# Kernel tuning notes

Hardware: AMD Instinct MI355X
Metric: run time of the kernel (lower is better)

The kernel has to match this reference:

```python
import jax, jax.numpy as jnp
import numpy as np

N, C_IN, C_OUT, K, B, EMB, GROUPS, EPS = 131072, 64, 64, 27, 8, 512, 32, 1e-5


def octree_group_norm(x, batch_id, gamma, beta):
    # Per-sample, per-group stats over all nodes of that sample (nempty=False).
    n, c = x.shape
    cpg = c // GROUPS
    xg = x.reshape(n, GROUPS, cpg)
    cnt = jax.ops.segment_sum(jnp.ones((n,), x.dtype), batch_id, num_segments=B)  # [B]
    s = jax.ops.segment_sum(xg.sum(-1), batch_id, num_segments=B)                 # [B,G]
    ss = jax.ops.segment_sum((xg * xg).sum(-1), batch_id, num_segments=B)         # [B,G]
    denom = (cnt * cpg)[:, None]
    mean = s / denom
    var = ss / denom - mean * mean
    xn = (xg - mean[batch_id][:, :, None]) * jax.lax.rsqrt(var[batch_id][:, :, None] + EPS)
    return xn.reshape(n, c) * gamma + beta


def octree_conv(x, neigh, W, b):
    # Sparse 27-neighbor gather conv: gather [N,27,Cin], contract with [27,Cin,Cout].
    gathered = x[neigh]                                   # [N,K,Cin]
    return jnp.einsum('nkc,kco->no', gathered, W) + b


def setup_inputs() -> dict:
    key = jax.random.key(0)
    ks = jax.random.split(key, 12)
    return {
        'x': jax.random.normal(ks[0], (N, C_IN), jnp.float32),
        'time_emb': jax.random.normal(ks[1], (B, EMB), jnp.float32),
        'batch_id': jnp.sort(jax.random.randint(ks[2], (N,), 0, B)),
        'neigh': jax.random.randint(ks[3], (N, K), 0, N),
        'gn1_gamma': jnp.ones((C_IN,), jnp.float32),
        'gn1_beta': jnp.zeros((C_IN,), jnp.float32),
        'W1': jax.random.normal(ks[4], (K, C_IN, C_OUT), jnp.float32) * 0.05,
        'b1': jax.random.normal(ks[5], (C_OUT,), jnp.float32) * 0.01,
        'Wt': jax.random.normal(ks[6], (EMB, C_OUT), jnp.float32) * 0.04,
        'bt': jnp.zeros((C_OUT,), jnp.float32),
        'gn2_gamma': jnp.ones((C_OUT,), jnp.float32),
        'gn2_beta': jnp.zeros((C_OUT,), jnp.float32),
        'W2': jax.random.normal(ks[7], (K, C_OUT, C_OUT), jnp.float32) * 0.05,
        'b2': jnp.zeros((C_OUT,), jnp.float32),
    }


def reference(x, time_emb, batch_id, neigh, gn1_gamma, gn1_beta, W1, b1,
              Wt, bt, gn2_gamma, gn2_beta, W2, b2):
    h = jax.nn.silu(octree_group_norm(x, batch_id, gn1_gamma, gn1_beta))
    h = octree_conv(h, neigh, W1, b1)
    # time embedding: SiLU -> Linear, scattered per-sample onto nodes
    t = jax.nn.silu(time_emb) @ Wt + bt                   # [B, Cout]
    h = h + t[batch_id]
    h = jax.nn.silu(octree_group_norm(h, batch_id, gn2_gamma, gn2_beta))
    h = octree_conv(h, neigh, W2, b2)
    return h + x  # res_conv is identity since dim_in == dim_out
```

## Files before the change

kernel.cpp:

```cpp
#include <hip/hip_runtime.h>
#include <hip/hip_bf16.h>
#include <cstdint>

typedef unsigned short u16;
typedef __attribute__((ext_vector_type(8))) __bf16 bf16x8;
typedef __attribute__((ext_vector_type(4))) float f32x4;

#define N_NODES 131072
#define C 64
#define KNB 27
#define BATCH 8
#define EMB 512
#define NGROUP 32
#define GN_EPS 1e-5f

__device__ __forceinline__ void gload_lds16(const void* gsrc, void* ldsdst) {
    __builtin_amdgcn_global_load_lds(
        (const __attribute__((address_space(1))) char*)(unsigned long long)(uintptr_t)gsrc,
        (__attribute__((address_space(3))) char*)(unsigned int)(uintptr_t)ldsdst,
        16, 0, 0);
}

__device__ __forceinline__ float silu_f(float x) {
    return x / (1.0f + __expf(-x));
}

__device__ __forceinline__ u16 f2bf(float x) {
    __hip_bfloat16 h = __float2bfloat16(x);
    return __builtin_bit_cast(u16, h);
}

__device__ __forceinline__ float bf2f(u16 h) {
    unsigned u = ((unsigned)h) << 16;
    return __builtin_bit_cast(float, u);
}

__device__ __forceinline__ unsigned pack2(float a, float b) {
    return (unsigned)f2bf(a) | ((unsigned)f2bf(b) << 16);
}

__global__ void setup_kernel(const float* __restrict__ W1, const float* __restrict__ W2,
                             u16* __restrict__ Wb1, u16* __restrict__ Wb2,
                             const float* __restrict__ te, const float* __restrict__ Wt,
                             const float* __restrict__ bt, float* __restrict__ tvec,
                             const float* __restrict__ x, const int* __restrict__ batch_id,
                             float* __restrict__ stats, float* __restrict__ cnt) {
    __shared__ float sh[520];
    const int bid = blockIdx.x;
    const int t = threadIdx.x;
    if (bid < 216) {
        const int per = KNB * C * C;
        int e0 = (bid * 256 + t) * 4;
#pragma unroll
        for (int d = 0; d < 4; ++d) {
            int idx = e0 + d;
            const float* src = (idx < per) ? W1 : W2;
            u16* dst = (idx < per) ? Wb1 : Wb2;
            int e = (idx < per) ? idx : idx - per;
            int k = e >> 12;
            int rem = e & 4095;
            int co = rem >> 6;
            int ci = rem & 63;
            dst[e] = f2bf(src[(k * C + ci) * C + co]);
        }
    } else if (bid < 224) {
        int b = bid - 216;
        int co = t & 63, seg = t >> 6;
        float acc = 0.f;
        for (int i = 0; i < 128; ++i) {
            int e = seg * 128 + i;
            float v = te[b * EMB + e];
            acc += silu_f(v) * Wt[e * C + co];
        }
        sh[t] = acc;
        __syncthreads();
        if (t < 64) tvec[b * C + t] = sh[t] + sh[t + 64] + sh[t + 128] + sh[t + 192] + bt[t];
    } else {
        for (int i = t; i < 520; i += 256) sh[i] = 0.f;
        __syncthreads();
        const int n0 = (bid - 224) * 256;
        const int c4 = t & 15, r = t >> 4;
        float s0 = 0.f, ss0 = 0.f, s1 = 0.f, ss1 = 0.f, c = 0.f;
        int cur = -1;
        for (int i = 0; i < 16; ++i) {
            int n = n0 + i * 16 + r;
            int b = batch_id[n];
            if (b != cur) {
                if (cur >= 0) {
                    int g0 = 2 * c4;
                    atomicAdd(&sh[(cur * NGROUP + g0) * 2 + 0], s0);
                    atomicAdd(&sh[(cur * NGROUP + g0) * 2 + 1], ss0);
                    atomicAdd(&sh[(cur * NGROUP + g0 + 1) * 2 + 0], s1);
                    atomicAdd(&sh[(cur * NGROUP + g0 + 1) * 2 + 1], ss1);
                    if (c4 == 0) atomicAdd(&sh[512 + cur], c);
                }
                cur = b; s0 = ss0 = s1 = ss1 = c = 0.f;
            }
            float4 v = *(const float4*)(x + (size_t)n * C + c4 * 4);
            s0 += v.x + v.y;  ss0 += v.x * v.x + v.y * v.y;
            s1 += v.z + v.w;  ss1 += v.z * v.z + v.w * v.w;
            c += 1.f;
        }
        {
            int g0 = 2 * c4;
            atomicAdd(&sh[(cur * NGROUP + g0) * 2 + 0], s0);
            atomicAdd(&sh[(cur * NGROUP + g0) * 2 + 1], ss0);
            atomicAdd(&sh[(cur * NGROUP + g0 + 1) * 2 + 0], s1);
            atomicAdd(&sh[(cur * NGROUP + g0 + 1) * 2 + 1], ss1);
            if (c4 == 0) atomicAdd(&sh[512 + cur], c);
        }
        __syncthreads();
        for (int i = t; i < 512; i += 256)
            if (sh[i] != 0.f) atomicAdd(&stats[i], sh[i]);
        if (t < 8 && sh[512 + t] != 0.f) atomicAdd(&cnt[t], sh[512 + t]);
    }
}

__global__ void gn_apply_f32(const float* __restrict__ x, const int* __restrict__ batch_id,
                             const float* __restrict__ stats, const float* __restrict__ cnt,
                             const float* __restrict__ gamma, const float* __restrict__ beta,
                             u16* __restrict__ out) {
    int idx = blockIdx.x * 256 + threadIdx.x;
    int n = idx >> 3, seg = idx & 7;
    int b = batch_id[n];
    float denom = cnt[b] * 2.0f;
    float4 v0 = *(const float4*)(x + (size_t)n * C + seg * 8);
    float4 v1 = *(const float4*)(x + (size_t)n * C + seg * 8 + 4);
    float4 ga0 = *(const float4*)(gamma + seg * 8);
    float4 ga1 = *(const float4*)(gamma + seg * 8 + 4);
    float4 be0 = *(const float4*)(beta + seg * 8);
    float4 be1 = *(const float4*)(beta + seg * 8 + 4);
    float mn[4], rs[4];
#pragma unroll
    for (int p = 0; p < 4; ++p) {
        float2 st = *(const float2*)(stats + (b * NGROUP + seg * 4 + p) * 2);
        float mean = st.x / denom;
        float var = st.y / denom - mean * mean;
        mn[p] = mean;
        rs[p] = rsqrtf(var + GN_EPS);
    }
    float y0 = silu_f((v0.x - mn[0]) * rs[0] * ga0.x + be0.x);
    float y1 = silu_f((v0.y - mn[0]) * rs[0] * ga0.y + be0.y);
    float y2 = silu_f((v0.z - mn[1]) * rs[1] * ga0.z + be0.z);
    float y3 = silu_f((v0.w - mn[1]) * rs[1] * ga0.w + be0.w);
    float y4 = silu_f((v1.x - mn[2]) * rs[2] * ga1.x + be1.x);
    float y5 = silu_f((v1.y - mn[2]) * rs[2] * ga1.y + be1.y);
    float y6 = silu_f((v1.z - mn[3]) * rs[3] * ga1.z + be1.z);
    float y7 = silu_f((v1.w - mn[3]) * rs[3] * ga1.w + be1.w);
    uint4 o;
    o.x = pack2(y0, y1); o.y = pack2(y2, y3); o.z = pack2(y4, y5); o.w = pack2(y6, y7);
    *(uint4*)(out + (size_t)n * C + seg * 8) = o;
}

__global__ void gn_apply_bf16(const u16* __restrict__ x, const int* __restrict__ batch_id,
                              const float* __restrict__ stats, const float* __restrict__ cnt,
                              const float* __restrict__ gamma, const float* __restrict__ beta,
                              u16* __restrict__ out) {
    int idx = blockIdx.x * 256 + threadIdx.x;
    int n = idx >> 3, seg = idx & 7;
    int b = batch_id[n];
    float denom = cnt[b] * 2.0f;
    uint4 u = *(const uint4*)(x + (size_t)n * C + seg * 8);
    float4 ga0 = *(const float4*)(gamma + seg * 8);
    float4 ga1 = *(const float4*)(gamma + seg * 8 + 4);
    float4 be0 = *(const float4*)(beta + seg * 8);
    float4 be1 = *(const float4*)(beta + seg * 8 + 4);
    float mn[4], rs[4];
#pragma unroll
    for (int p = 0; p < 4; ++p) {
        float2 st = *(const float2*)(stats + (b * NGROUP + seg * 4 + p) * 2);
        float mean = st.x / denom;
        float var = st.y / denom - mean * mean;
        mn[p] = mean;
        rs[p] = rsqrtf(var + GN_EPS);
    }
    float v0 = bf2f(u.x & 0xffff), v1 = bf2f(u.x >> 16);
    float v2 = bf2f(u.y & 0xffff), v3 = bf2f(u.y >> 16);
    float v4 = bf2f(u.z & 0xffff), v5 = bf2f(u.z >> 16);
    float v6 = bf2f(u.w & 0xffff), v7 = bf2f(u.w >> 16);
    float y0 = silu_f((v0 - mn[0]) * rs[0] * ga0.x + be0.x);
    float y1 = silu_f((v1 - mn[0]) * rs[0] * ga0.y + be0.y);
    float y2 = silu_f((v2 - mn[1]) * rs[1] * ga0.z + be0.z);
    float y3 = silu_f((v3 - mn[1]) * rs[1] * ga0.w + be0.w);
    float y4 = silu_f((v4 - mn[2]) * rs[2] * ga1.x + be1.x);
    float y5 = silu_f((v5 - mn[2]) * rs[2] * ga1.y + be1.y);
    float y6 = silu_f((v6 - mn[3]) * rs[3] * ga1.z + be1.z);
    float y7 = silu_f((v7 - mn[3]) * rs[3] * ga1.w + be1.w);
    uint4 o;
    o.x = pack2(y0, y1); o.y = pack2(y2, y3); o.z = pack2(y4, y5); o.w = pack2(y6, y7);
    *(uint4*)(out + (size_t)n * C + seg * 8) = o;
}

template <bool ADD_T, bool FUSE_STATS, bool OUT_F32_RES>
__global__ __launch_bounds__(512, 4) void conv_kernel(
    const u16* __restrict__ act, const int* __restrict__ neigh,
    const u16* __restrict__ Wb, const float* __restrict__ bias,
    const float* __restrict__ tvec, const int* __restrict__ batch_id,
    const float* __restrict__ resid, void* __restrict__ outp,
    float* __restrict__ stats, float* __restrict__ cnt) {
    __shared__ u16 Wbuf[5 * 64 * 64];
    float* shs = (float*)Wbuf;

    const int tid = threadIdx.x;
    const int w = tid >> 6, lane = tid & 63;
    const int q = lane >> 4, m = lane & 15;
    const int n0 = blockIdx.x * 256;
    const int nw = n0 + w * 32;

    const int* nrow0 = neigh + (size_t)(nw + m) * KNB;
    const int* nrow1 = neigh + (size_t)(nw + 16 + m) * KNB;

    f32x4 acc[2][4] = {};
    bf16x8 aC[2][2];
    int offn0, offn1;

    {
        int o0 = nrow0[0] * C, o1 = nrow1[0] * C;
        aC[0][0] = *(const bf16x8*)(act + o0 + q * 8);
        aC[0][1] = *(const bf16x8*)(act + o0 + 32 + q * 8);
        aC[1][0] = *(const bf16x8*)(act + o1 + q * 8);
        aC[1][1] = *(const bf16x8*)(act + o1 + 32 + q * 8);
        offn0 = nrow0[1] * C;
        offn1 = nrow1[1] * C;
    }

    for (int phase = 0; phase < 6; ++phase) {
        const int k0 = phase * 5;
        const int nk = (phase == 5) ? 2 : 5;
        if (phase) __syncthreads();
        const int total = nk * 512;
#pragma unroll
        for (int it = 0; it < 5; ++it) {
            int cb = it * 512 + w * 64;
            if (cb < total) {
                int c = cb + lane;
                int r = c >> 3;
                int pos = c & 7;
                int srcc = pos ^ (r & 7);
                gload_lds16(Wb + (((k0 << 6) + r) << 6) + (srcc << 3), Wbuf + cb * 8);
            }
        }
        __syncthreads();

        for (int sI = 0; sI < nk; ++sI) {
            const int k = k0 + sI;
            const int kn = k + 1;
            bf16x8 an[2][2];
            if (kn < KNB) {
                an[0][0] = *(const bf16x8*)(act + offn0 + q * 8);
                an[0][1] = *(const bf16x8*)(act + offn0 + 32 + q * 8);
                an[1][0] = *(const bf16x8*)(act + offn1 + q * 8);
                an[1][1] = *(const bf16x8*)(act + offn1 + 32 + q * 8);
            }
            if (kn + 1 < KNB) {
                offn0 = nrow0[kn + 1] * C;
                offn1 = nrow1[kn + 1] * C;
            }
            const u16* wsl = Wbuf + sI * 4096;
#pragma unroll
            for (int kk = 0; kk < 2; ++kk) {
#pragma unroll
                for (int j = 0; j < 4; ++j) {
                    const int co = j * 16 + m;
                    const int lc = kk * 4 + q;
                    bf16x8 b = *(const bf16x8*)(wsl + (co << 6) + ((lc ^ (co & 7)) << 3));
                    acc[0][j] = __builtin_amdgcn_mfma_f32_16x16x32_bf16(aC[0][kk], b, acc[0][j], 0, 0, 0);
                    acc[1][j] = __builtin_amdgcn_mfma_f32_16x16x32_bf16(aC[1][kk], b, acc[1][j], 0, 0, 0);
                }
            }
            if (kn < KNB) {
                aC[0][0] = an[0][0]; aC[0][1] = an[0][1];
                aC[1][0] = an[1][0]; aC[1][1] = an[1][1];
            }
        }
    }

    float bs[4];
#pragma unroll
    for (int j = 0; j < 4; ++j) bs[j] = bias[j * 16 + m];

#pragma unroll
    for (int s = 0; s < 2; ++s) {
#pragma unroll
        for (int reg = 0; reg < 4; ++reg) {
            const int n = nw + s * 16 + q * 4 + reg;
            int b = 0;
            if (ADD_T) b = batch_id[n];
#pragma unroll
            for (int j = 0; j < 4; ++j) {
                const int co = j * 16 + m;
                float v = acc[s][j][reg] + bs[j];
                if (ADD_T) v += tvec[b * C + co];
                acc[s][j][reg] = v;
                if (OUT_F32_RES) {
                    ((float*)outp)[(size_t)n * C + co] = v + resid[(size_t)n * C + co];
                } else {
                    ((u16*)outp)[(size_t)n * C + co] = f2bf(v);
                }
            }
        }
    }

    if (FUSE_STATS) {
        __syncthreads();
        for (int i = tid; i < 520; i += 512) shs[i] = 0.f;
        __syncthreads();
        const int blo = batch_id[nw], bhi = batch_id[nw + 31];
        if (blo == bhi) {
#pragma unroll
            for (int j = 0; j < 4; ++j) {
                float s = 0.f, ss = 0.f;
#pragma unroll
                for (int sq = 0; sq < 2; ++sq)
#pragma unroll
                    for (int reg = 0; reg < 4; ++reg) {
                        float v = acc[sq][j][reg];
                        s += v; ss += v * v;
                    }
                s += __shfl_xor(s, 16, 64);  ss += __shfl_xor(ss, 16, 64);
                s += __shfl_xor(s, 32, 64);  ss += __shfl_xor(ss, 32, 64);
                s += __shfl_xor(s, 1, 64);   ss += __shfl_xor(ss, 1, 64);
                if (q == 0 && (m & 1) == 0) {
                    int g = (j * 16 + m) >> 1;
                    atomicAdd(&shs[(blo * NGROUP + g) * 2 + 0], s);
                    atomicAdd(&shs[(blo * NGROUP + g) * 2 + 1], ss);
                }
            }
        } else {
#pragma unroll
            for (int sq = 0; sq < 2; ++sq)
#pragma unroll
                for (int reg = 0; reg < 4; ++reg) {
                    int b = batch_id[nw + sq * 16 + q * 4 + reg];
#pragma unroll
                    for (int j = 0; j < 4; ++j) {
                        int g = (j * 16 + m) >> 1;
                        float v = acc[sq][j][reg];
                        atomicAdd(&shs[(b * NGROUP + g) * 2 + 0], v);
                        atomicAdd(&shs[(b * NGROUP + g) * 2 + 1], v * v);
                    }
                }
        }
        if (tid < 256) atomicAdd(&shs[512 + batch_id[n0 + tid]], 1.0f);
        __syncthreads();
        if (tid < 512 && shs[tid] != 0.f) atomicAdd(&stats[tid], shs[tid]);
        if (tid < 8 && shs[512 + tid] != 0.f) atomicAdd(&cnt[tid], shs[512 + tid]);
    }
}

extern "C" void kernel_launch(void* const* d_in, const int* in_sizes, int n_in,
                              void* d_out, int out_size, void* d_ws, size_t ws_size,
                              hipStream_t stream) {
    const float* x        = (const float*)d_in[0];
    const float* time_emb = (const float*)d_in[1];
    const int*   batch_id = (const int*)d_in[2];
    const int*   neigh    = (const int*)d_in[3];
    const float* g1       = (const float*)d_in[4];
    const float* be1      = (const float*)d_in[5];
    const float* W1       = (const float*)d_in[6];
    const float* b1       = (const float*)d_in[7];
    const float* Wt       = (const float*)d_in[8];
    const float* bt       = (const float*)d_in[9];
    const float* g2       = (const float*)d_in[10];
    const float* be2      = (const float*)d_in[11];
    const float* W2       = (const float*)d_in[12];
    const float* b2       = (const float*)d_in[13];

    char* ws = (char*)d_ws;
    u16*   h1     = (u16*)(ws + 0);
    u16*   h2     = (u16*)(ws + 16777216);
    u16*   h3     = (u16*)(ws + 33554432);
    u16*   Wb1    = (u16*)(ws + 50331648);
    u16*   Wb2    = (u16*)(ws + 50552832);
    float* tvec   = (float*)(ws + 50774016);
    float* stats1 = (float*)(ws + 50776064);
    float* cnt1   = stats1 + 512;
    float* stats2 = cnt1 + 8;
    float* cnt2   = stats2 + 512;

    hipMemsetAsync(ws + 50776064, 0, 1040 * sizeof(float), stream);
    setup_kernel<<<736, 256, 0, stream>>>(W1, W2, Wb1, Wb2, time_emb, Wt, bt, tvec,
                                          x, batch_id, stats1, cnt1);
    gn_apply_f32<<<4096, 256, 0, stream>>>(x, batch_id, stats1, cnt1, g1, be1, h1);
    conv_kernel<true, true, false><<<512, 512, 0, stream>>>(
        h1, neigh, Wb1, b1, tvec, batch_id, nullptr, (void*)h2, stats2, cnt2);
    gn_apply_bf16<<<4096, 256, 0, stream>>>(h2, batch_id, stats2, cnt2, g2, be2, h3);
    conv_kernel<false, false, true><<<512, 512, 0, stream>>>(
        h3, neigh, Wb2, b2, nullptr, nullptr, x, (void*)d_out, nullptr, nullptr);
}
```

Before: 302.6 us.

## Fuse all stages into one persistent kernel with grid barriers

Replaces the five separate launches (setup, two GN applies, two convs) with a single persistent 512-block kernel. Stages are separated by software grid barriers built on atomic counters. The conv gather is also deepened from double to triple-buffered register prefetch, with 6-tap weight phases and full unrolling. This removes launch gaps and inter-kernel drains, but relies on all 512 blocks being co-resident, adds spin-wait barrier costs, and raises register and LDS pressure.

Result: slower. 621.4 us (+105.4%).

```diff
diff --git a/kernel.cpp b/kernel.cpp
--- a/kernel.cpp
+++ b/kernel.cpp
@@ -6,13 +6,13 @@
 typedef __attribute__((ext_vector_type(8))) __bf16 bf16x8;
 typedef __attribute__((ext_vector_type(4))) float f32x4;
 
-#define N_NODES 131072
+#define NN 131072
 #define C 64
 #define KNB 27
-#define BATCH 8
 #define EMB 512
 #define NGROUP 32
 #define GN_EPS 1e-5f
+#define NBLK 512
 
 __device__ __forceinline__ void gload_lds16(const void* gsrc, void* ldsdst) {
     __builtin_amdgcn_global_load_lds(
@@ -39,168 +39,46 @@
     return (unsigned)f2bf(a) | ((unsigned)f2bf(b) << 16);
 }
 
-__global__ void setup_kernel(const float* __restrict__ W1, const float* __restrict__ W2,
-                             u16* __restrict__ Wb1, u16* __restrict__ Wb2,
-                             const float* __restrict__ te, const float* __restrict__ Wt,
-                             const float* __restrict__ bt, float* __restrict__ tvec,
-                             const float* __restrict__ x, const int* __restrict__ batch_id,
-                             float* __restrict__ stats, float* __restrict__ cnt) {
-    __shared__ float sh[520];
-    const int bid = blockIdx.x;
-    const int t = threadIdx.x;
-    if (bid < 216) {
-        const int per = KNB * C * C;
-        int e0 = (bid * 256 + t) * 4;
-#pragma unroll
-        for (int d = 0; d < 4; ++d) {
-            int idx = e0 + d;
-            const float* src = (idx < per) ? W1 : W2;
-            u16* dst = (idx < per) ? Wb1 : Wb2;
-            int e = (idx < per) ? idx : idx - per;
-            int k = e >> 12;
-            int rem = e & 4095;
-            int co = rem >> 6;
-            int ci = rem & 63;
-            dst[e] = f2bf(src[(k * C + ci) * C + co]);
-        }
-    } else if (bid < 224) {
-        int b = bid - 216;
-        int co = t & 63, seg = t >> 6;
-        float acc = 0.f;
-        for (int i = 0; i < 128; ++i) {
-            int e = seg * 128 + i;
-            float v = te[b * EMB + e];
-            acc += silu_f(v) * Wt[e * C + co];
-        }
-        sh[t] = acc;
-        __syncthreads();
-        if (t < 64) tvec[b * C + t] = sh[t] + sh[t + 64] + sh[t + 128] + sh[t + 192] + bt[t];
-    } else {
-        for (int i = t; i < 520; i += 256) sh[i] = 0.f;
-        __syncthreads();
-        const int n0 = (bid - 224) * 256;
-        const int c4 = t & 15, r = t >> 4;
-        float s0 = 0.f, ss0 = 0.f, s1 = 0.f, ss1 = 0.f, c = 0.f;
-        int cur = -1;
-        for (int i = 0; i < 16; ++i) {
-            int n = n0 + i * 16 + r;
-            int b = batch_id[n];
-            if (b != cur) {
-                if (cur >= 0) {
-                    int g0 = 2 * c4;
-                    atomicAdd(&sh[(cur * NGROUP + g0) * 2 + 0], s0);
-                    atomicAdd(&sh[(cur * NGROUP + g0) * 2 + 1], ss0);
-                    atomicAdd(&sh[(cur * NGROUP + g0 + 1) * 2 + 0], s1);
-                    atomicAdd(&sh[(cur * NGROUP + g0 + 1) * 2 + 1], ss1);
-                    if (c4 == 0) atomicAdd(&sh[512 + cur], c);
-                }
-                cur = b; s0 = ss0 = s1 = ss1 = c = 0.f;
-            }
-            float4 v = *(const float4*)(x + (size_t)n * C + c4 * 4);
-            s0 += v.x + v.y;  ss0 += v.x * v.x + v.y * v.y;
-            s1 += v.z + v.w;  ss1 += v.z * v.z + v.w * v.w;
-            c += 1.f;
-        }
-        {
-            int g0 = 2 * c4;
-            atomicAdd(&sh[(cur * NGROUP + g0) * 2 + 0], s0);
-            atomicAdd(&sh[(cur * NGROUP + g0) * 2 + 1], ss0);
-            atomicAdd(&sh[(cur * NGROUP + g0 + 1) * 2 + 0], s1);
-            atomicAdd(&sh[(cur * NGROUP + g0 + 1) * 2 + 1], ss1);
-            if (c4 == 0) atomicAdd(&sh[512 + cur], c);
-        }
-        __syncthreads();
-        for (int i = t; i < 512; i += 256)
-            if (sh[i] != 0.f) atomicAdd(&stats[i], sh[i]);
-        if (t < 8 && sh[512 + t] != 0.f) atomicAdd(&cnt[t], sh[512 + t]);
-    }
-}
-
-__global__ void gn_apply_f32(const float* __restrict__ x, const int* __restrict__ batch_id,
-                             const float* __restrict__ stats, const float* __restrict__ cnt,
-                             const float* __restrict__ gamma, const float* __restrict__ beta,
-                             u16* __restrict__ out) {
-    int idx = blockIdx.x * 256 + threadIdx.x;
-    int n = idx >> 3, seg = idx & 7;
-    int b = batch_id[n];
-    float denom = cnt[b] * 2.0f;
-    float4 v0 = *(const float4*)(x + (size_t)n * C + seg * 8);
-    float4 v1 = *(const float4*)(x + (size_t)n * C + seg * 8 + 4);
-    float4 ga0 = *(const float4*)(gamma + seg * 8);
-    float4 ga1 = *(const float4*)(gamma + seg * 8 + 4);
-    float4 be0 = *(const float4*)(beta + seg * 8);
-    float4 be1 = *(const float4*)(beta + seg * 8 + 4);
-    float mn[4], rs[4];
-#pragma unroll
-    for (int p = 0; p < 4; ++p) {
-        float2 st = *(const float2*)(stats + (b * NGROUP + seg * 4 + p) * 2);
-        float mean = st.x / denom;
-        float var = st.y / denom - mean * mean;
-        mn[p] = mean;
-        rs[p] = rsqrtf(var + GN_EPS);
-    }
-    float y0 = silu_f((v0.x - mn[0]) * rs[0] * ga0.x + be0.x);
-    float y1 = silu_f((v0.y - mn[0]) * rs[0] * ga0.y + be0.y);
-    float y2 = silu_f((v0.z - mn[1]) * rs[1] * ga0.z + be0.z);
-    float y3 = silu_f((v0.w - mn[1]) * rs[1] * ga0.w + be0.w);
-    float y4 = silu_f((v1.x - mn[2]) * rs[2] * ga1.x + be1.x);
-    float y5 = silu_f((v1.y - mn[2]) * rs[2] * ga1.y + be1.y);
-    float y6 = silu_f((v1.z - mn[3]) * rs[3] * ga1.z + be1.z);
-    float y7 = silu_f((v1.w - mn[3]) * rs[3] * ga1.w + be1.w);
-    uint4 o;
-    o.x = pack2(y0, y1); o.y = pack2(y2, y3); o.z = pack2(y4, y5); o.w = pack2(y6, y7);
-    *(uint4*)(out + (size_t)n * C + seg * 8) = o;
-}
-
-__global__ void gn_apply_bf16(const u16* __restrict__ x, const int* __restrict__ batch_id,
-                              const float* __restrict__ stats, const float* __restrict__ cnt,
-                              const float* __restrict__ gamma, const float* __restrict__ beta,
-                              u16* __restrict__ out) {
-    int idx = blockIdx.x * 256 + threadIdx.x;
-    int n = idx >> 3, seg = idx & 7;
-    int b = batch_id[n];
-    float denom = cnt[b] * 2.0f;
-    uint4 u = *(const uint4*)(x + (size_t)n * C + seg * 8);
-    float4 ga0 = *(const float4*)(gamma + seg * 8);
-    float4 ga1 = *(const float4*)(gamma + seg * 8 + 4);
-    float4 be0 = *(const float4*)(beta + seg * 8);
-    float4 be1 = *(const float4*)(beta + seg * 8 + 4);
-    float mn[4], rs[4];
-#pragma unroll
-    for (int p = 0; p < 4; ++p) {
-        float2 st = *(const float2*)(stats + (b * NGROUP + seg * 4 + p) * 2);
-        float mean = st.x / denom;
-        float var = st.y / denom - mean * mean;
-        mn[p] = mean;
-        rs[p] = rsqrtf(var + GN_EPS);
-    }
-    float v0 = bf2f(u.x & 0xffff), v1 = bf2f(u.x >> 16);
-    float v2 = bf2f(u.y & 0xffff), v3 = bf2f(u.y >> 16);
-    float v4 = bf2f(u.z & 0xffff), v5 = bf2f(u.z >> 16);
-    float v6 = bf2f(u.w & 0xffff), v7 = bf2f(u.w >> 16);
-    float y0 = silu_f((v0 - mn[0]) * rs[0] * ga0.x + be0.x);
-    float y1 = silu_f((v1 - mn[0]) * rs[0] * ga0.y + be0.y);
-    float y2 = silu_f((v2 - mn[1]) * rs[1] * ga0.z + be0.z);
-    float y3 = silu_f((v3 - mn[1]) * rs[1] * ga0.w + be0.w);
-    float y4 = silu_f((v4 - mn[2]) * rs[2] * ga1.x + be1.x);
-    float y5 = silu_f((v5 - mn[2]) * rs[2] * ga1.y + be1.y);
-    float y6 = silu_f((v6 - mn[3]) * rs[3] * ga1.z + be1.z);
-    float y7 = silu_f((v7 - mn[3]) * rs[3] * ga1.w + be1.w);
-    uint4 o;
-    o.x = pack2(y0, y1); o.y = pack2(y2, y3); o.z = pack2(y4, y5); o.w = pack2(y6, y7);
-    *(uint4*)(out + (size_t)n * C + seg * 8) = o;
-}
+__device__ __forceinline__ void grid_barrier(unsigned* ctr) {
+    __syncthreads();
+    if (threadIdx.x == 0) {
+        __threadfence();
+        __hip_atomic_fetch_add(ctr, 1u, __ATOMIC_ACQ_REL, __HIP_MEMORY_SCOPE_AGENT);
+        while (__hip_atomic_load(ctr, __ATOMIC_ACQUIRE, __HIP_MEMORY_SCOPE_AGENT) < NBLK) {
+            __builtin_amdgcn_s_sleep(16);
+        }
+        __threadfence();
+    }
+    __syncthreads();
+}
+
+struct MegaArgs {
+    const float* x;
+    const float* time_emb;
+    const int* batch_id;
+    const int* neigh;
+    const float* g1; const float* be1;
+    const float* W1; const float* b1;
+    const float* Wt; const float* bt;
+    const float* g2; const float* be2;
+    const float* W2; const float* b2;
+    u16* Wb1; u16* Wb2;
+    float* tvec;
+    float* stats1; float* cnt1;
+    float* stats2; float* cnt2;
+    unsigned* bar;
+    u16* h1; u16* h2; u16* h3;
+    float* out;
+};
 
 template <bool ADD_T, bool FUSE_STATS, bool OUT_F32_RES>
-__global__ __launch_bounds__(512, 4) void conv_kernel(
+__device__ __forceinline__ void conv_body(
     const u16* __restrict__ act, const int* __restrict__ neigh,
     const u16* __restrict__ Wb, const float* __restrict__ bias,
     const float* __restrict__ tvec, const int* __restrict__ batch_id,
     const float* __restrict__ resid, void* __restrict__ outp,
-    float* __restrict__ stats, float* __restrict__ cnt) {
-    __shared__ u16 Wbuf[5 * 64 * 64];
+    float* __restrict__ stats, float* __restrict__ cnt, u16* Wbuf) {
     float* shs = (float*)Wbuf;
-
     const int tid = threadIdx.x;
     const int w = tid >> 6, lane = tid & 63;
     const int q = lane >> 4, m = lane & 15;
@@ -211,50 +89,57 @@
     const int* nrow1 = neigh + (size_t)(nw + 16 + m) * KNB;
 
     f32x4 acc[2][4] = {};
-    bf16x8 aC[2][2];
+    bf16x8 aB[3][2][2];
     int offn0, offn1;
 
     {
         int o0 = nrow0[0] * C, o1 = nrow1[0] * C;
-        aC[0][0] = *(const bf16x8*)(act + o0 + q * 8);
-        aC[0][1] = *(const bf16x8*)(act + o0 + 32 + q * 8);
-        aC[1][0] = *(const bf16x8*)(act + o1 + q * 8);
-        aC[1][1] = *(const bf16x8*)(act + o1 + 32 + q * 8);
-        offn0 = nrow0[1] * C;
-        offn1 = nrow1[1] * C;
-    }
-
-    for (int phase = 0; phase < 6; ++phase) {
-        const int k0 = phase * 5;
-        const int nk = (phase == 5) ? 2 : 5;
+        aB[0][0][0] = *(const bf16x8*)(act + o0 + q * 8);
+        aB[0][0][1] = *(const bf16x8*)(act + o0 + 32 + q * 8);
+        aB[0][1][0] = *(const bf16x8*)(act + o1 + q * 8);
+        aB[0][1][1] = *(const bf16x8*)(act + o1 + 32 + q * 8);
+        o0 = nrow0[1] * C; o1 = nrow1[1] * C;
+        aB[1][0][0] = *(const bf16x8*)(act + o0 + q * 8);
+        aB[1][0][1] = *(const bf16x8*)(act + o0 + 32 + q * 8);
+        aB[1][1][0] = *(const bf16x8*)(act + o1 + q * 8);
+        aB[1][1][1] = *(const bf16x8*)(act + o1 + 32 + q * 8);
+        offn0 = nrow0[2] * C;
+        offn1 = nrow1[2] * C;
+    }
+
+#pragma unroll
+    for (int phase = 0; phase < 5; ++phase) {
+        const int k0 = phase * 6;
+        const int nk = (phase == 4) ? 3 : 6;
         if (phase) __syncthreads();
         const int total = nk * 512;
 #pragma unroll
-        for (int it = 0; it < 5; ++it) {
+        for (int it = 0; it < 6; ++it) {
             int cb = it * 512 + w * 64;
             if (cb < total) {
-                int c = cb + lane;
-                int r = c >> 3;
-                int pos = c & 7;
-                int srcc = pos ^ (r & 7);
-                gload_lds16(Wb + (((k0 << 6) + r) << 6) + (srcc << 3), Wbuf + cb * 8);
-            }
-        }
-        __syncthreads();
-
+                int cc = cb + lane;
+                int rr = cc >> 3;
+                int pos = cc & 7;
+                int srcc = pos ^ (rr & 7);
+                gload_lds16(Wb + (((k0 << 6) + rr) << 6) + (srcc << 3), Wbuf + cb * 8);
+            }
+        }
+        __syncthreads();
+
+#pragma unroll
         for (int sI = 0; sI < nk; ++sI) {
             const int k = k0 + sI;
-            const int kn = k + 1;
-            bf16x8 an[2][2];
-            if (kn < KNB) {
-                an[0][0] = *(const bf16x8*)(act + offn0 + q * 8);
-                an[0][1] = *(const bf16x8*)(act + offn0 + 32 + q * 8);
-                an[1][0] = *(const bf16x8*)(act + offn1 + q * 8);
-                an[1][1] = *(const bf16x8*)(act + offn1 + 32 + q * 8);
-            }
-            if (kn + 1 < KNB) {
-                offn0 = nrow0[kn + 1] * C;
-                offn1 = nrow1[kn + 1] * C;
+            const int use = sI % 3;
+            const int nxt = (sI + 2) % 3;
+            if (k + 2 < KNB) {
+                aB[nxt][0][0] = *(const bf16x8*)(act + offn0 + q * 8);
+                aB[nxt][0][1] = *(const bf16x8*)(act + offn0 + 32 + q * 8);
+                aB[nxt][1][0] = *(const bf16x8*)(act + offn1 + q * 8);
+                aB[nxt][1][1] = *(const bf16x8*)(act + offn1 + 32 + q * 8);
+            }
+            if (k + 3 < KNB) {
+                offn0 = nrow0[k + 3] * C;
+                offn1 = nrow1[k + 3] * C;
             }
             const u16* wsl = Wbuf + sI * 4096;
 #pragma unroll
@@ -264,13 +149,9 @@
                     const int co = j * 16 + m;
                     const int lc = kk * 4 + q;
                     bf16x8 b = *(const bf16x8*)(wsl + (co << 6) + ((lc ^ (co & 7)) << 3));
-                    acc[0][j] = __builtin_amdgcn_mfma_f32_16x16x32_bf16(aC[0][kk], b, acc[0][j], 0, 0, 0);
-                    acc[1][j] = __builtin_amdgcn_mfma_f32_16x16x32_bf16(aC[1][kk], b, acc[1][j], 0, 0, 0);
+                    acc[0][j] = __builtin_amdgcn_mfma_f32_16x16x32_bf16(aB[use][0][kk], b, acc[0][j], 0, 0, 0);
+                    acc[1][j] = __builtin_amdgcn_mfma_f32_16x16x32_bf16(aB[use][1][kk], b, acc[1][j], 0, 0, 0);
                 }
-            }
-            if (kn < KNB) {
-                aC[0][0] = an[0][0]; aC[0][1] = an[0][1];
-                aC[1][0] = an[1][0]; aC[1][1] = an[1][1];
             }
         }
     }
@@ -348,43 +229,213 @@
     }
 }
 
+__device__ __forceinline__ void gn_apply_f32_body(
+    const float* __restrict__ x, const int* __restrict__ batch_id,
+    const float* __restrict__ stats, const float* __restrict__ cnt,
+    const float* __restrict__ gamma, const float* __restrict__ beta,
+    u16* __restrict__ out) {
+    const int gstride = NBLK * 512;
+    for (int idx = blockIdx.x * 512 + threadIdx.x; idx < NN * 8; idx += gstride) {
+        int n = idx >> 3, seg = idx & 7;
+        int b = batch_id[n];
+        float denom = cnt[b] * 2.0f;
+        float4 v0 = *(const float4*)(x + (size_t)n * C + seg * 8);
+        float4 v1 = *(const float4*)(x + (size_t)n * C + seg * 8 + 4);
+        float4 ga0 = *(const float4*)(gamma + seg * 8);
+        float4 ga1 = *(const float4*)(gamma + seg * 8 + 4);
+        float4 be0 = *(const float4*)(beta + seg * 8);
+        float4 be1 = *(const float4*)(beta + seg * 8 + 4);
+        float mn[4], rs[4];
+#pragma unroll
+        for (int p = 0; p < 4; ++p) {
+            float2 st = *(const float2*)(stats + (b * NGROUP + seg * 4 + p) * 2);
+            float mean = st.x / denom;
+            float var = st.y / denom - mean * mean;
+            mn[p] = mean;
+            rs[p] = rsqrtf(var + GN_EPS);
+        }
+        float y0 = silu_f((v0.x - mn[0]) * rs[0] * ga0.x + be0.x);
+        float y1 = silu_f((v0.y - mn[0]) * rs[0] * ga0.y + be0.y);
+        float y2 = silu_f((v0.z - mn[1]) * rs[1] * ga0.z + be0.z);
+        float y3 = silu_f((v0.w - mn[1]) * rs[1] * ga0.w + be0.w);
+        float y4 = silu_f((v1.x - mn[2]) * rs[2] * ga1.x + be1.x);
+        float y5 = silu_f((v1.y - mn[2]) * rs[2] * ga1.y + be1.y);
+        float y6 = silu_f((v1.z - mn[3]) * rs[3] * ga1.z + be1.z);
+        float y7 = silu_f((v1.w - mn[3]) * rs[3] * ga1.w + be1.w);
+        uint4 o;
+        o.x = pack2(y0, y1); o.y = pack2(y2, y3); o.z = pack2(y4, y5); o.w = pack2(y6, y7);
+        *(uint4*)(out + (size_t)n * C + seg * 8) = o;
+    }
+}
+
+__device__ __forceinline__ void gn_apply_bf16_body(
+    const u16* __restrict__ x, const int* __restrict__ batch_id,
+    const float* __restrict__ stats, const float* __restrict__ cnt,
+    const float* __restrict__ gamma, const float* __restrict__ beta,
+    u16* __restrict__ out) {
+    const int gstride = NBLK * 512;
+    for (int idx = blockIdx.x * 512 + threadIdx.x; idx < NN * 8; idx += gstride) {
+        int n = idx >> 3, seg = idx & 7;
+        int b = batch_id[n];
+        float denom = cnt[b] * 2.0f;
+        uint4 u = *(const uint4*)(x + (size_t)n * C + seg * 8);
+        float4 ga0 = *(const float4*)(gamma + seg * 8);
+        float4 ga1 = *(const float4*)(gamma + seg * 8 + 4);
+        float4 be0 = *(const float4*)(beta + seg * 8);
+        float4 be1 = *(const float4*)(beta + seg * 8 + 4);
+        float mn[4], rs[4];
+#pragma unroll
+        for (int p = 0; p < 4; ++p) {
+            float2 st = *(const float2*)(stats + (b * NGROUP + seg * 4 + p) * 2);
+            float mean = st.x / denom;
+            float var = st.y / denom - mean * mean;
+            mn[p] = mean;
+            rs[p] = rsqrtf(var + GN_EPS);
+        }
+        float v0 = bf2f(u.x & 0xffff), v1 = bf2f(u.x >> 16);
+        float v2 = bf2f(u.y & 0xffff), v3 = bf2f(u.y >> 16);
+        float v4 = bf2f(u.z & 0xffff), v5 = bf2f(u.z >> 16);
+        float v6 = bf2f(u.w & 0xffff), v7 = bf2f(u.w >> 16);
+        float y0 = silu_f((v0 - mn[0]) * rs[0] * ga0.x + be0.x);
+        float y1 = silu_f((v1 - mn[0]) * rs[0] * ga0.y + be0.y);
+        float y2 = silu_f((v2 - mn[1]) * rs[1] * ga0.z + be0.z);
+        float y3 = silu_f((v3 - mn[1]) * rs[1] * ga0.w + be0.w);
+        float y4 = silu_f((v4 - mn[2]) * rs[2] * ga1.x + be1.x);
+        float y5 = silu_f((v5 - mn[2]) * rs[2] * ga1.y + be1.y);
+        float y6 = silu_f((v6 - mn[3]) * rs[3] * ga1.z + be1.z);
+        float y7 = silu_f((v7 - mn[3]) * rs[3] * ga1.w + be1.w);
+        uint4 o;
+        o.x = pack2(y0, y1); o.y = pack2(y2, y3); o.z = pack2(y4, y5); o.w = pack2(y6, y7);
+        *(uint4*)(out + (size_t)n * C + seg * 8) = o;
+    }
+}
+
+__global__ __launch_bounds__(512, 4) void mega_kernel(MegaArgs a) {
+    __shared__ u16 Wbuf[6 * 64 * 64];
+    float* shf = (float*)Wbuf;
+    const int bid = blockIdx.x;
+    const int t = threadIdx.x;
+
+    if (bid < 108) {
+        const int per = KNB * C * C;
+        int e0 = (bid * 512 + t) * 4;
+#pragma unroll
+        for (int d = 0; d < 4; ++d) {
+            int idx = e0 + d;
+            const float* src = (idx < per) ? a.W1 : a.W2;
+            u16* dst = (idx < per) ? a.Wb1 : a.Wb2;
+            int e = (idx < per) ? idx : idx - per;
+            int k = e >> 12;
+            int rem = e & 4095;
+            int co = rem >> 6;
+            int ci = rem & 63;
+            dst[e] = f2bf(src[(k * C + ci) * C + co]);
+        }
+    } else if (bid < 116) {
+        int b = bid - 108;
+        int co = t & 63, seg = t >> 6;
+        float acc = 0.f;
+        for (int i = 0; i < 64; ++i) {
+            int e = seg * 64 + i;
+            float v = a.time_emb[b * EMB + e];
+            acc += silu_f(v) * a.Wt[e * C + co];
+        }
+        shf[t] = acc;
+        __syncthreads();
+        if (t < 64) {
+            float s = a.bt[t];
+#pragma unroll
+            for (int j = 0; j < 8; ++j) s += shf[t + 64 * j];
+            a.tvec[b * C + t] = s;
+        }
+    }
+    __syncthreads();
+    {
+        for (int i = t; i < 520; i += 512) shf[i] = 0.f;
+        __syncthreads();
+        const int n0s = bid * 256;
+        const int c4 = t & 15, r = t >> 4;
+        float s0 = 0.f, ss0 = 0.f, s1 = 0.f, ss1 = 0.f, c = 0.f;
+        int cur = -1;
+        for (int i = 0; i < 8; ++i) {
+            int n = n0s + i * 32 + r;
+            int b = a.batch_id[n];
+            if (b != cur) {
+                if (cur >= 0) {
+                    int g0 = 2 * c4;
+                    atomicAdd(&shf[(cur * NGROUP + g0) * 2 + 0], s0);
+                    atomicAdd(&shf[(cur * NGROUP + g0) * 2 + 1], ss0);
+                    atomicAdd(&shf[(cur * NGROUP + g0 + 1) * 2 + 0], s1);
+                    atomicAdd(&shf[(cur * NGROUP + g0 + 1) * 2 + 1], ss1);
+                    if (c4 == 0) atomicAdd(&shf[512 + cur], c);
+                }
+                cur = b; s0 = ss0 = s1 = ss1 = c = 0.f;
+            }
+            float4 v = *(const float4*)(a.x + (size_t)n * C + c4 * 4);
+            s0 += v.x + v.y;  ss0 += v.x * v.x + v.y * v.y;
+            s1 += v.z + v.w;  ss1 += v.z * v.z + v.w * v.w;
+            c += 1.f;
+        }
+        {
+            int g0 = 2 * c4;
+            atomicAdd(&shf[(cur * NGROUP + g0) * 2 + 0], s0);
+            atomicAdd(&shf[(cur * NGROUP + g0) * 2 + 1], ss0);
+            atomicAdd(&shf[(cur * NGROUP + g0 + 1) * 2 + 0], s1);
+            atomicAdd(&shf[(cur * NGROUP + g0 + 1) * 2 + 1], ss1);
+            if (c4 == 0) atomicAdd(&shf[512 + cur], c);
+        }
+        __syncthreads();
+        if (t < 512 && shf[t] != 0.f) atomicAdd(&a.stats1[t], shf[t]);
+        if (t < 8 && shf[512 + t] != 0.f) atomicAdd(&a.cnt1[t], shf[512 + t]);
+    }
+
+    grid_barrier(a.bar + 0);
+    gn_apply_f32_body(a.x, a.batch_id, a.stats1, a.cnt1, a.g1, a.be1, a.h1);
+
+    grid_barrier(a.bar + 16);
+    conv_body<true, true, false>(a.h1, a.neigh, a.Wb1, a.b1, a.tvec, a.batch_id,
+                                 nullptr, (void*)a.h2, a.stats2, a.cnt2, Wbuf);
+
+    grid_barrier(a.bar + 32);
+    gn_apply_bf16_body(a.h2, a.batch_id, a.stats2, a.cnt2, a.g2, a.be2, a.h3);
+
+    grid_barrier(a.bar + 48);
+    conv_body<false, false, true>(a.h3, a.neigh, a.Wb2, a.b2, nullptr, a.batch_id,
+                                  a.x, (void*)a.out, nullptr, nullptr, Wbuf);
+}
+
 extern "C" void kernel_launch(void* const* d_in, const int* in_sizes, int n_in,
                               void* d_out, int out_size, void* d_ws, size_t ws_size,
                               hipStream_t stream) {
-    const float* x        = (const float*)d_in[0];
-    const float* time_emb = (const float*)d_in[1];
-    const int*   batch_id = (const int*)d_in[2];
-    const int*   neigh    = (const int*)d_in[3];
-    const float* g1       = (const float*)d_in[4];
-    const float* be1      = (const float*)d_in[5];
-    const float* W1       = (const float*)d_in[6];
-    const float* b1       = (const float*)d_in[7];
-    const float* Wt       = (const float*)d_in[8];
-    const float* bt       = (const float*)d_in[9];
-    const float* g2       = (const float*)d_in[10];
-    const float* be2      = (const float*)d_in[11];
-    const float* W2       = (const float*)d_in[12];
-    const float* b2       = (const float*)d_in[13];
-
     char* ws = (char*)d_ws;
-    u16*   h1     = (u16*)(ws + 0);
-    u16*   h2     = (u16*)(ws + 16777216);
-    u16*   h3     = (u16*)(ws + 33554432);
-    u16*   Wb1    = (u16*)(ws + 50331648);
-    u16*   Wb2    = (u16*)(ws + 50552832);
-    float* tvec   = (float*)(ws + 50774016);
-    float* stats1 = (float*)(ws + 50776064);
-    float* cnt1   = stats1 + 512;
-    float* stats2 = cnt1 + 8;
-    float* cnt2   = stats2 + 512;
-
-    hipMemsetAsync(ws + 50776064, 0, 1040 * sizeof(float), stream);
-    setup_kernel<<<736, 256, 0, stream>>>(W1, W2, Wb1, Wb2, time_emb, Wt, bt, tvec,
-                                          x, batch_id, stats1, cnt1);
-    gn_apply_f32<<<4096, 256, 0, stream>>>(x, batch_id, stats1, cnt1, g1, be1, h1);
-    conv_kernel<true, true, false><<<512, 512, 0, stream>>>(
-        h1, neigh, Wb1, b1, tvec, batch_id, nullptr, (void*)h2, stats2, cnt2);
-    gn_apply_bf16<<<4096, 256, 0, stream>>>(h2, batch_id, stats2, cnt2, g2, be2, h3);
-    conv_kernel<false, false, true><<<512, 512, 0, stream>>>(
-        h3, neigh, Wb2, b2, nullptr, nullptr, x, (void*)d_out, nullptr, nullptr);
-}
+    MegaArgs a;
+    a.x        = (const float*)d_in[0];
+    a.time_emb = (const float*)d_in[1];
+    a.batch_id = (const int*)d_in[2];
+    a.neigh    = (const int*)d_in[3];
+    a.g1       = (const float*)d_in[4];
+    a.be1      = (const float*)d_in[5];
+    a.W1       = (const float*)d_in[6];
+    a.b1       = (const float*)d_in[7];
+    a.Wt       = (const float*)d_in[8];
+    a.bt       = (const float*)d_in[9];
+    a.g2       = (const float*)d_in[10];
+    a.be2      = (const float*)d_in[11];
+    a.W2       = (const float*)d_in[12];
+    a.b2       = (const float*)d_in[13];
+    a.h1     = (u16*)(ws + 0);
+    a.h2     = (u16*)(ws + 16777216);
+    a.h3     = (u16*)(ws + 33554432);
+    a.Wb1    = (u16*)(ws + 50331648);
+    a.Wb2    = (u16*)(ws + 50552832);
+    a.tvec   = (float*)(ws + 50774016);
+    a.stats1 = (float*)(ws + 50776064);
+    a.cnt1   = a.stats1 + 512;
+    a.stats2 = a.cnt1 + 8;
+    a.cnt2   = a.stats2 + 512;
+    a.bar    = (unsigned*)(ws + 50780224);
+    a.out    = (float*)d_out;
+
+    hipMemsetAsync(ws + 50776064, 0, 4416, stream);
+    mega_kernel<<<NBLK, 512, 0, stream>>>(a);
+}
```
